# Kernel tuning notes

Measured on AMD Instinct MI355X. Metric: run time of the kernel, lower is better.

The kernel has to match this reference:

```python
import jax, jax.numpy as jnp
import numpy as np

N_EVENT = 100000
N_TRACE = 20000
E_EE = 1000000
E_ET = 500000
E_TE = 500000
D = 128          # embedding_dim == hidden_dim
OUT = 64         # output_dim
L = 3            # num_layers
NTYPES_EDGES = 3 # edge types
B = 64           # graphs per batch


def setup_inputs() -> dict:
    key = jax.random.key(0)
    ks = jax.random.split(key, 16)
    s = 1.0 / np.sqrt(D)
    inp = {
        "event_ids": jnp.arange(N_EVENT, dtype=jnp.int64 if jax.config.jax_enable_x64 else jnp.int32),
        "trace_ids": jnp.arange(N_TRACE, dtype=jnp.int64 if jax.config.jax_enable_x64 else jnp.int32),
        "e2e_src": jax.random.randint(ks[0], (E_EE,), 0, N_EVENT),
        "e2e_dst": jax.random.randint(ks[1], (E_EE,), 0, N_EVENT),
        "e2t_src": jax.random.randint(ks[2], (E_ET,), 0, N_EVENT),
        "e2t_dst": jax.random.randint(ks[3], (E_ET,), 0, N_TRACE),
        "t2e_src": jax.random.randint(ks[4], (E_TE,), 0, N_TRACE),
        "t2e_dst": jax.random.randint(ks[5], (E_TE,), 0, N_EVENT),
        "event_batch": jnp.sort(jax.random.randint(ks[6], (N_EVENT,), 0, B)),
        "trace_batch": jnp.sort(jax.random.randint(ks[7], (N_TRACE,), 0, B)),
        # learned parameters
        "emb_event": jax.random.normal(ks[8], (N_EVENT, D), jnp.float32),
        "emb_trace": jax.random.normal(ks[9], (N_TRACE, D), jnp.float32),
        # per-layer, per-edge-type SAGEConv weights: lin_l (neighbor, with bias), lin_r (root, no bias)
        "Wl": jax.random.normal(ks[10], (L, NTYPES_EDGES, D, D), jnp.float32) * s,
        "bl": jnp.zeros((L, NTYPES_EDGES, D), jnp.float32),
        "Wr": jax.random.normal(ks[11], (L, NTYPES_EDGES, D, D), jnp.float32) * s,
        # output MLP head
        "W1": jax.random.normal(ks[12], (D, D), jnp.float32) * s,
        "b1": jnp.zeros((D,), jnp.float32),
        "W2": jax.random.normal(ks[13], (OUT, D), jnp.float32) * s,
        "b2": jnp.zeros((OUT,), jnp.float32),
    }
    return inp


def reference(event_ids, trace_ids, e2e_src, e2e_dst, e2t_src, e2t_dst,
              t2e_src, t2e_dst, event_batch, trace_batch,
              emb_event, emb_trace, Wl, bl, Wr, W1, b1, W2, b2):
    def seg_mean(x_src, src, dst, n_dst):
        # mean-aggregate source features onto destination nodes (SAGEConv default aggr)
        s = jax.ops.segment_sum(x_src[src], dst, num_segments=n_dst)
        c = jax.ops.segment_sum(jnp.ones(dst.shape, x_src.dtype), dst, num_segments=n_dst)
        return s / jnp.maximum(c, 1.0)[:, None]

    # per-node-type embedding lookup
    x = {"event": emb_event[event_ids], "trace": emb_trace[trace_ids]}
    n = {"event": event_ids.shape[0], "trace": trace_ids.shape[0]}
    # edge types: (src_type, dst_type, src_idx, dst_idx), conv index matches Wl/bl/Wr axis 1
    edges = [
        ("event", "event", e2e_src, e2e_dst),
        ("event", "trace", e2t_src, e2t_dst),
        ("trace", "event", t2e_src, t2e_dst),
    ]
    n_layers = Wl.shape[0]
    for l in range(n_layers):
        new = {k: jnp.zeros((n[k], Wl.shape[-2]), x[k].dtype) for k in x}
        for i, (st, dt, s_idx, d_idx) in enumerate(edges):
            m = seg_mean(x[st], s_idx, d_idx, n[dt])
            # SAGEConv: lin_l(mean neighbors) + lin_r(root); HeteroConv aggr='sum' across edge types
            new[dt] = new[dt] + m @ Wl[l, i].T + bl[l, i] + x[dt] @ Wr[l, i].T
        x = new
    # global_add_pool per node type, then stack+sum over node types
    pooled = (jax.ops.segment_sum(x["event"], event_batch, num_segments=B)
              + jax.ops.segment_sum(x["trace"], trace_batch, num_segments=B))
    h = jax.nn.relu(pooled @ W1.T + b1)
    return h @ W2.T + b2
```

## Files before the change

### kernel.cpp

```cpp
#include <hip/hip_runtime.h>
#include <hip/hip_bf16.h>


#define D 128
#define NB 64
#define OUTD 64
#define NLAY 3

typedef __bf16 bf16;
typedef __bf16 bf16x4 __attribute__((ext_vector_type(4)));
typedef __bf16 bf16x8 __attribute__((ext_vector_type(8)));
typedef float  f32x16 __attribute__((ext_vector_type(16)));

#define LOAD16_TO_LDS(gp, lp) \
    __builtin_amdgcn_global_load_lds((const __attribute__((address_space(1))) void*)(gp), \
                                     (__attribute__((address_space(3))) void*)(lp), 16, 0, 0)

__global__ void gather_all(const float* __restrict__ embE, const int* __restrict__ idsE,
                           bf16* __restrict__ xE, int nE,
                           const float* __restrict__ embT, const int* __restrict__ idsT,
                           bf16* __restrict__ xT, int nT) {
    int idx = blockIdx.x * blockDim.x + threadIdx.x;
    const float* emb; const int* ids; bf16* x;
    int tE = nE * 32;
    if (idx < tE) { emb = embE; ids = idsE; x = xE; }
    else {
        idx -= tE;
        if (idx >= nT * 32) return;
        emb = embT; ids = idsT; x = xT;
    }
    int r = idx >> 5, v = idx & 31;
    float4 f = ((const float4*)(emb + (size_t)ids[r] * D))[v];
    bf16x4 o;
    o[0] = (bf16)f.x; o[1] = (bf16)f.y; o[2] = (bf16)f.z; o[3] = (bf16)f.w;
    ((bf16x4*)(x + (size_t)r * D))[v] = o;
}

__global__ void hist_all(const int* __restrict__ dEE, const int* __restrict__ dET,
                         const int* __restrict__ dTE, int nEE, int nET, int nTE,
                         int* __restrict__ degEE, int* __restrict__ degET, int* __restrict__ degTE,
                         int* __restrict__ rkEE, int* __restrict__ rkET, int* __restrict__ rkTE) {
    int e = blockIdx.x * blockDim.x + threadIdx.x;
    const int* dst; int* deg; int* rk;
    if (e < nEE) { dst = dEE; deg = degEE; rk = rkEE; }
    else {
        e -= nEE;
        if (e < nET) { dst = dET; deg = degET; rk = rkET; }
        else {
            e -= nET;
            if (e >= nTE) return;
            dst = dTE; deg = degTE; rk = rkTE;
        }
    }
    rk[e] = atomicAdd(&deg[dst[e]], 1);
}

__global__ void scan_p1_all(const int* __restrict__ dA, int* __restrict__ oA, int* __restrict__ sA, int nA,
                            const int* __restrict__ dB, int* __restrict__ oB, int* __restrict__ sB, int nB,
                            const int* __restrict__ dC, int* __restrict__ oC, int* __restrict__ sC, int nC) {
    int nbA = (nA + 1023) >> 10, nbB = (nB + 1023) >> 10;
    int b = blockIdx.x;
    const int* deg; int* off; int* bsum; int n; int lb;
    if (b < nbA) { deg = dA; off = oA; bsum = sA; n = nA; lb = b; }
    else if (b < nbA + nbB) { deg = dB; off = oB; bsum = sB; n = nB; lb = b - nbA; }
    else { deg = dC; off = oC; bsum = sC; n = nC; lb = b - nbA - nbB; }
    __shared__ int s[256];
    int t = threadIdx.x;
    int base = lb * 1024 + t * 4;
    int v[4];
    #pragma unroll
    for (int i = 0; i < 4; ++i) v[i] = (base + i < n) ? deg[base + i] : 0;
    int tot = v[0] + v[1] + v[2] + v[3];
    s[t] = tot;
    __syncthreads();
    for (int st = 1; st < 256; st <<= 1) {
        int x = (t >= st) ? s[t - st] : 0;
        __syncthreads();
        s[t] += x;
        __syncthreads();
    }
    int run = s[t] - tot;
    #pragma unroll
    for (int i = 0; i < 4; ++i) {
        if (base + i < n) off[base + i] = run;
        run += v[i];
    }
    if (t == 255) bsum[lb] = s[255];
}

__global__ void scan_p2_all(int* __restrict__ sA, int nbA,
                            int* __restrict__ sB, int nbB,
                            int* __restrict__ sC, int nbC) {
    int* bsum; int nb;
    if (blockIdx.x == 0) { bsum = sA; nb = nbA; }
    else if (blockIdx.x == 1) { bsum = sB; nb = nbB; }
    else { bsum = sC; nb = nbC; }
    __shared__ int s[256];
    int t = threadIdx.x;
    int v = (t < nb) ? bsum[t] : 0;
    s[t] = v;
    __syncthreads();
    for (int st = 1; st < 256; st <<= 1) {
        int x = (t >= st) ? s[t - st] : 0;
        __syncthreads();
        s[t] += x;
        __syncthreads();
    }
    if (t < nb) bsum[t] = s[t] - v;
    if (t == 0) bsum[nb] = s[255];
}

__global__ void scan_p3_all(int* __restrict__ oA, const int* __restrict__ sA, int nA,
                            int* __restrict__ oB, const int* __restrict__ sB, int nB,
                            int* __restrict__ oC, const int* __restrict__ sC, int nC) {
    int cbA = (nA + 255) >> 8, cbB = (nB + 255) >> 8;
    int b = blockIdx.x;
    int* off; const int* bsum; int n; int lb;
    if (b < cbA) { off = oA; bsum = sA; n = nA; lb = b; }
    else if (b < cbA + cbB) { off = oB; bsum = sB; n = nB; lb = b - cbA; }
    else { off = oC; bsum = sC; n = nC; lb = b - cbA - cbB; }
    int i = lb * 256 + threadIdx.x;
    if (i < n) off[i] += bsum[i >> 10];
    if (i == 0) off[n] = bsum[(n + 1023) >> 10];
}

__global__ void adj_fill_all(const int* __restrict__ sEE, const int* __restrict__ dEE, int nEE,
                             const int* __restrict__ sET, const int* __restrict__ dET, int nET,
                             const int* __restrict__ sTE, const int* __restrict__ dTE, int nTE,
                             const int* __restrict__ oEE, const int* __restrict__ oET,
                             const int* __restrict__ oTE,
                             const int* __restrict__ rkEE, const int* __restrict__ rkET,
                             const int* __restrict__ rkTE,
                             int* __restrict__ adjEE, int* __restrict__ adjET,
                             int* __restrict__ adjTE) {
    int e = blockIdx.x * blockDim.x + threadIdx.x;
    const int* src; const int* dst; const int* off; const int* rk; int* adj;
    if (e < nEE) { src = sEE; dst = dEE; off = oEE; rk = rkEE; adj = adjEE; }
    else {
        e -= nEE;
        if (e < nET) { src = sET; dst = dET; off = oET; rk = rkET; adj = adjET; }
        else {
            e -= nET;
            if (e >= nTE) return;
            src = sTE; dst = dTE; off = oTE; rk = rkTE; adj = adjTE;
        }
    }
    adj[off[dst[e]] + rk[e]] = src[e];
}

__global__ void agg_all(const bf16* __restrict__ xE, const bf16* __restrict__ xT,
                        const int* __restrict__ offEE, const int* __restrict__ adjEE,
                        const int* __restrict__ offTE, const int* __restrict__ adjTE,
                        const int* __restrict__ offET, const int* __restrict__ adjET,
                        bf16* __restrict__ mEE, bf16* __restrict__ mTE, bf16* __restrict__ mET,
                        int nE, int nT) {
    int gw = (blockIdx.x * blockDim.x + threadIdx.x) >> 6;
    int lane = threadIdx.x & 63;
    int qE = (nE + 3) >> 2, qT = (nT + 3) >> 2;
    const bf16* xsrc; const int* off; const int* adj; bf16* out; int ndst;
    if (gw < qE) { xsrc = xE; off = offEE; adj = adjEE; out = mEE; ndst = nE; }
    else if (gw < 2 * qE) { gw -= qE; xsrc = xT; off = offTE; adj = adjTE; out = mTE; ndst = nE; }
    else {
        gw -= 2 * qE;
        if (gw >= qT) return;
        xsrc = xE; off = offET; adj = adjET; out = mET; ndst = nT;
    }
    int sub = lane >> 4;
    int sl  = lane & 15;
    int row = gw * 4 + sub;
    if (row >= ndst) row = ndst - 1;
    int s0 = off[row], s1 = off[row + 1];
    float a[8] = {};
    int j = s0;
    for (; j + 8 <= s1; j += 8) {
        int ii[8];
        #pragma unroll
        for (int u = 0; u < 8; ++u) ii[u] = adj[j + u];
        bf16x8 v[8];
        #pragma unroll
        for (int u = 0; u < 8; ++u) v[u] = ((const bf16x8*)(xsrc + (size_t)ii[u] * D))[sl];
        #pragma unroll
        for (int u = 0; u < 8; ++u)
            #pragma unroll
            for (int e = 0; e < 8; ++e) a[e] += (float)v[u][e];
    }
    for (; j + 4 <= s1; j += 4) {
        int i0 = adj[j], i1 = adj[j + 1], i2 = adj[j + 2], i3 = adj[j + 3];
        bf16x8 v0 = ((const bf16x8*)(xsrc + (size_t)i0 * D))[sl];
        bf16x8 v1 = ((const bf16x8*)(xsrc + (size_t)i1 * D))[sl];
        bf16x8 v2 = ((const bf16x8*)(xsrc + (size_t)i2 * D))[sl];
        bf16x8 v3 = ((const bf16x8*)(xsrc + (size_t)i3 * D))[sl];
        #pragma unroll
        for (int e = 0; e < 8; ++e)
            a[e] += (float)v0[e] + (float)v1[e] + (float)v2[e] + (float)v3[e];
    }
    for (; j < s1; ++j) {
        int i0 = adj[j];
        bf16x8 v0 = ((const bf16x8*)(xsrc + (size_t)i0 * D))[sl];
        #pragma unroll
        for (int e = 0; e < 8; ++e) a[e] += (float)v0[e];
    }
    float inv = 1.0f / fmaxf((float)(s1 - s0), 1.0f);
    bf16x8 o;
    #pragma unroll
    for (int e = 0; e < 8; ++e) o[e] = (bf16)(a[e] * inv);
    ((bf16x8*)(out + (size_t)row * D))[sl] = o;
}

__global__ void prep_weights_packed(const float* __restrict__ Wl, const float* __restrict__ Wr,
                                    bf16* __restrict__ wbuf) {
    int idx = blockIdx.x * blockDim.x + threadIdx.x;
    if (idx >= NLAY * 5 * 2048) return;
    int l = idx / (5 * 2048);
    int rem = idx - l * 5 * 2048;
    int mat = rem >> 11;
    int q = rem & 2047;
    int lane = q & 63, t = (q >> 6) & 7, w = q >> 9;
    int r = w * 32 + (lane & 31);
    int c = t * 16 + (lane >> 5) * 8;
    size_t l3 = (size_t)l * 3;
    const float* s0;
    const float* s1 = nullptr;
    switch (mat) {
        case 0: s0 = Wl + (l3 + 0) * D * D; break;
        case 1: s0 = Wl + (l3 + 2) * D * D; break;
        case 2: s0 = Wr + (l3 + 0) * D * D; s1 = Wr + (l3 + 2) * D * D; break;
        case 3: s0 = Wl + (l3 + 1) * D * D; break;
        default: s0 = Wr + (l3 + 1) * D * D; break;
    }
    bf16x8 hi, lo;
    #pragma unroll
    for (int e = 0; e < 8; ++e) {
        float v = s0[r * D + c + e];
        if (s1) v += s1[r * D + c + e];
        bf16 h = (bf16)v;
        hi[e] = h;
        lo[e] = (bf16)(v - (float)h);
    }
    bf16* base = wbuf + (size_t)l * 10 * D * D;
    ((bf16x8*)(base + (size_t)(2 * mat) * D * D))[q] = hi;
    ((bf16x8*)(base + (size_t)(2 * mat + 1) * D * D))[q] = lo;
}

__global__ void prep_bias(const float* __restrict__ bl, float* __restrict__ bbuf) {
    int idx = blockIdx.x * blockDim.x + threadIdx.x;
    if (idx >= NLAY * D) return;
    int l = idx >> 7, o = idx & (D - 1);
    bbuf[l * 2 * D + o]     = bl[(size_t)(l * 3 + 0) * D + o] + bl[(size_t)(l * 3 + 2) * D + o];
    bbuf[l * 2 * D + D + o] = bl[(size_t)(l * 3 + 1) * D + o];
}

__device__ __forceinline__ void gemm_body(const bf16* A0, const bf16* A1, const bf16* A2,
                                          const bf16* Wp, const float* bias, bf16* out,
                                          int M, int nm, int row0, bf16* As) {
    int tid = threadIdx.x;
    int wave = tid >> 6, lane = tid & 63;
    int m = lane & 31, half = lane >> 5;

    f32x16 acc[2];
    #pragma unroll
    for (int rt = 0; rt < 2; ++rt)
        #pragma unroll
        for (int i = 0; i < 16; ++i) acc[rt][i] = 0.f;

    const bf16* Aptr[3] = {A0, A1, A2};
    #pragma unroll
    for (int s = 0; s < 3; ++s) {
        if (s >= nm) break;
        if (s) __syncthreads();
        const bf16* Amat = Aptr[s];
        #pragma unroll
        for (int p = 0; p < 4; ++p) {
            int si = p * 256 + tid;
            int r = si >> 4, u = si & 15;
            int gr = row0 + r; if (gr >= M) gr = M - 1;
            int gc = (u ^ (r & 15)) * 8;
            LOAD16_TO_LDS(Amat + (size_t)gr * D + gc, As + (size_t)(p * 4 + wave) * 512);
        }
        const bf16* wph = Wp + (size_t)(2 * s) * D * D + ((size_t)wave * 512 + lane) * 8;
        const bf16* wpl = wph + D * D;
        bf16x8 bh_c  = *(const bf16x8*)(wph);
        bf16x8 blo_c = *(const bf16x8*)(wpl);
        __syncthreads();

        #pragma unroll 1
        for (int t = 0; t < 8; ++t) {
            bf16x8 bh_n, blo_n;
            if (t < 7) {
                bh_n  = *(const bf16x8*)(wph + (t + 1) * 512);
                blo_n = *(const bf16x8*)(wpl + (t + 1) * 512);
            }
            bf16x8 af[2];
            #pragma unroll
            for (int rt = 0; rt < 2; ++rt) {
                int r = rt * 32 + m;
                int c = t * 2 + half;
                af[rt] = *(const bf16x8*)(As + ((size_t)r * 16 + (c ^ (r & 15))) * 8);
            }
            acc[0] = __builtin_amdgcn_mfma_f32_32x32x16_bf16(af[0], bh_c,  acc[0], 0, 0, 0);
            acc[1] = __builtin_amdgcn_mfma_f32_32x32x16_bf16(af[1], bh_c,  acc[1], 0, 0, 0);
            acc[0] = __builtin_amdgcn_mfma_f32_32x32x16_bf16(af[0], blo_c, acc[0], 0, 0, 0);
            acc[1] = __builtin_amdgcn_mfma_f32_32x32x16_bf16(af[1], blo_c, acc[1], 0, 0, 0);
            bh_c = bh_n; blo_c = blo_n;
        }
    }

    int col = wave * 32 + m;
    float bv = bias[col];
    #pragma unroll
    for (int rt = 0; rt < 2; ++rt) {
        #pragma unroll
        for (int r = 0; r < 16; ++r) {
            int row = row0 + rt * 32 + (r & 3) + 8 * (r >> 2) + 4 * half;
            if (row < M) out[(size_t)row * D + col] = (bf16)(acc[rt][r] + bv);
        }
    }
}

__global__ __launch_bounds__(256) void gemm_all(const bf16* __restrict__ eA0, const bf16* __restrict__ eA1,
                                                const bf16* __restrict__ eA2, const bf16* __restrict__ eW,
                                                const float* __restrict__ eB, bf16* __restrict__ eOut,
                                                int Me, int bE,
                                                const bf16* __restrict__ tA0, const bf16* __restrict__ tA1,
                                                const bf16* __restrict__ tW, const float* __restrict__ tB,
                                                bf16* __restrict__ tOut, int Mt) {
    __shared__ bf16 As[64 * 128];
    if ((int)blockIdx.x < bE)
        gemm_body(eA0, eA1, eA2, eW, eB, eOut, Me, 3, blockIdx.x * 64, As);
    else
        gemm_body(tA0, tA1, (const bf16*)nullptr, tW, tB, tOut, Mt, 2,
                  ((int)blockIdx.x - bE) * 64, As);
}

__global__ void pool_all(const bf16* __restrict__ xE, const int* __restrict__ bEv, int nE, int pbE,
                         const bf16* __restrict__ xT, const int* __restrict__ bTr, int nT,
                         float* __restrict__ pooled) {
    int c = threadIdx.x;
    int blk = blockIdx.x;
    const bf16* x; const int* batch; int n, r0;
    if (blk < pbE) { x = xE; batch = bEv; n = nE; r0 = blk * 64; }
    else { x = xT; batch = bTr; n = nT; r0 = (blk - pbE) * 64; }
    int r1 = min(r0 + 64, n);
    if (r0 >= r1) return;
    int cur = batch[r0];
    float acc = 0.f;
    for (int r = r0; r < r1; ++r) {
        int b = batch[r];
        if (b != cur) { atomicAdd(&pooled[cur * D + c], acc); acc = 0.f; cur = b; }
        acc += (float)x[(size_t)r * D + c];
    }
    atomicAdd(&pooled[cur * D + c], acc);
}

__global__ void head_kernel(const float* __restrict__ pooled, const float* __restrict__ W1,
                            const float* __restrict__ b1, const float* __restrict__ W2,
                            const float* __restrict__ b2, float* __restrict__ out) {
    __shared__ float p[D];
    __shared__ float h[D];
    int b = blockIdx.x, t = threadIdx.x;
    p[t] = pooled[b * D + t];
    __syncthreads();
    float s = b1[t];
    const float* w = W1 + (size_t)t * D;
    #pragma unroll 4
    for (int k = 0; k < D; ++k) s += p[k] * w[k];
    h[t] = fmaxf(s, 0.f);
    __syncthreads();
    if (t < OUTD) {
        float s2 = b2[t];
        const float* w2 = W2 + (size_t)t * D;
        #pragma unroll 4
        for (int k = 0; k < D; ++k) s2 += h[k] * w2[k];
        out[b * OUTD + t] = s2;
    }
}

extern "C" void kernel_launch(void* const* d_in, const int* in_sizes, int n_in,
                              void* d_out, int out_size, void* d_ws, size_t ws_size,
                              hipStream_t stream) {
    const int* event_ids   = (const int*)d_in[0];
    const int* trace_ids   = (const int*)d_in[1];
    const int* e2e_src     = (const int*)d_in[2];
    const int* e2e_dst     = (const int*)d_in[3];
    const int* e2t_src     = (const int*)d_in[4];
    const int* e2t_dst     = (const int*)d_in[5];
    const int* t2e_src     = (const int*)d_in[6];
    const int* t2e_dst     = (const int*)d_in[7];
    const int* event_batch = (const int*)d_in[8];
    const int* trace_batch = (const int*)d_in[9];
    const float* emb_event = (const float*)d_in[10];
    const float* emb_trace = (const float*)d_in[11];
    const float* Wl        = (const float*)d_in[12];
    const float* bl        = (const float*)d_in[13];
    const float* Wr        = (const float*)d_in[14];
    const float* W1        = (const float*)d_in[15];
    const float* b1        = (const float*)d_in[16];
    const float* W2        = (const float*)d_in[17];
    const float* b2        = (const float*)d_in[18];

    const int NE = in_sizes[0];
    const int NT = in_sizes[1];
    const int EE = in_sizes[2];
    const int ET = in_sizes[4];
    const int TE = in_sizes[6];

    size_t cur = 0;
    auto alloc = [&](size_t bytes) -> void* {
        cur = (cur + 255) & ~(size_t)255;
        void* p = (char*)d_ws + cur;
        cur += bytes;
        return p;
    };
    bf16* x_event   = (bf16*)alloc((size_t)NE * D * 2);
    bf16* x_trace   = (bf16*)alloc((size_t)NT * D * 2);
    bf16* nx_event  = (bf16*)alloc((size_t)NE * D * 2);
    bf16* nx_trace  = (bf16*)alloc((size_t)NT * D * 2);
    bf16* m_ee      = (bf16*)alloc((size_t)NE * D * 2);
    bf16* m_te      = (bf16*)alloc((size_t)NE * D * 2);
    bf16* m_et      = (bf16*)alloc((size_t)NT * D * 2);
    float* pooled   = (float*)alloc((size_t)NB * D * 4);
    bf16* wbuf      = (bf16*)alloc((size_t)NLAY * 10 * D * D * 2);
    float* bbuf     = (float*)alloc((size_t)NLAY * 2 * D * 4);
    int* zbase  = (int*)alloc(((size_t)NE + NT + NE) * 4);
    int* deg_ee = zbase;
    int* deg_et = deg_ee + NE;
    int* deg_te = deg_et + NT;
    int* off_ee = (int*)alloc((size_t)(NE + 1) * 4);
    int* adj_ee = (int*)alloc((size_t)EE * 4);
    int* off_et = (int*)alloc((size_t)(NT + 1) * 4);
    int* adj_et = (int*)alloc((size_t)ET * 4);
    int* off_te = (int*)alloc((size_t)(NE + 1) * 4);
    int* adj_te = (int*)alloc((size_t)TE * 4);
    int* bsum_ee = (int*)alloc(((size_t)(NE + 1023) / 1024 + 1) * 4);
    int* bsum_et = (int*)alloc(((size_t)(NT + 1023) / 1024 + 1) * 4);
    int* bsum_te = (int*)alloc(((size_t)(NE + 1023) / 1024 + 1) * 4);
    int* rk_ee = (int*)m_ee;
    int* rk_et = (int*)m_te;
    int* rk_te = (int*)m_et;
    (void)ws_size; (void)n_in; (void)out_size;

    const int nbE = (NE + 1023) / 1024;
    const int nbT = (NT + 1023) / 1024;

    hipMemsetAsync(zbase, 0, ((size_t)NE + NT + NE) * 4, stream);

    gather_all<<<((NE + NT) * 32 + 255) / 256, 256, 0, stream>>>(
        emb_event, event_ids, x_event, NE, emb_trace, trace_ids, x_trace, NT);

    prep_weights_packed<<<(NLAY * 5 * 2048 + 255) / 256, 256, 0, stream>>>(Wl, Wr, wbuf);
    prep_bias<<<(NLAY * D + 255) / 256, 256, 0, stream>>>(bl, bbuf);

    hist_all<<<(EE + ET + TE + 255) / 256, 256, 0, stream>>>(
        e2e_dst, e2t_dst, t2e_dst, EE, ET, TE,
        deg_ee, deg_et, deg_te, rk_ee, rk_et, rk_te);
    scan_p1_all<<<nbE + nbT + nbE, 256, 0, stream>>>(
        deg_ee, off_ee, bsum_ee, NE, deg_et, off_et, bsum_et, NT, deg_te, off_te, bsum_te, NE);
    scan_p2_all<<<3, 256, 0, stream>>>(bsum_ee, nbE, bsum_et, nbT, bsum_te, nbE);
    scan_p3_all<<<((NE + 255) >> 8) * 2 + ((NT + 255) >> 8), 256, 0, stream>>>(
        off_ee, bsum_ee, NE, off_et, bsum_et, NT, off_te, bsum_te, NE);
    adj_fill_all<<<(EE + ET + TE + 255) / 256, 256, 0, stream>>>(
        e2e_src, e2e_dst, EE, e2t_src, e2t_dst, ET, t2e_src, t2e_dst, TE,
        off_ee, off_et, off_te, rk_ee, rk_et, rk_te, adj_ee, adj_et, adj_te);

    const int qE = (NE + 3) >> 2, qT = (NT + 3) >> 2;
    const int aggBlocks = (2 * qE + qT + 3) / 4;
    const int bE = (NE + 63) / 64, bT = (NT + 63) / 64;
    for (int l = 0; l < NLAY; ++l) {
        const bf16* wl_ev = wbuf + (size_t)l * 10 * D * D;
        const bf16* wl_tr = wl_ev + (size_t)6 * D * D;
        const float* be = bbuf + (size_t)l * 2 * D;
        const float* bt = be + D;

        agg_all<<<aggBlocks, 256, 0, stream>>>(x_event, x_trace,
                                               off_ee, adj_ee, off_te, adj_te, off_et, adj_et,
                                               m_ee, m_te, m_et, NE, NT);
        gemm_all<<<bE + bT, 256, 0, stream>>>(m_ee, m_te, x_event, wl_ev, be, nx_event, NE, bE,
                                              m_et, x_trace, wl_tr, bt, nx_trace, NT);

        bf16* t;
        t = x_event; x_event = nx_event; nx_event = t;
        t = x_trace; x_trace = nx_trace; nx_trace = t;
    }

    hipMemsetAsync(pooled, 0, (size_t)NB * D * 4, stream);
    const int pbE = (NE + 63) / 64, pbT = (NT + 63) / 64;
    pool_all<<<pbE + pbT, D, 0, stream>>>(x_event, event_batch, NE, pbE,
                                          x_trace, trace_batch, NT, pooled);

    head_kernel<<<NB, D, 0, stream>>>(pooled, W1, b1, W2, b2, (float*)d_out);
}
```

Measured before the change: 660.3 us.

## Fold last-layer linear transform into pooling via linearity of sum-pool

```diff
diff --git a/kernel.cpp b/kernel.cpp
--- a/kernel.cpp
+++ b/kernel.cpp
@@ -145,7 +145,7 @@
             src = sTE; dst = dTE; off = oTE; rk = rkTE; adj = adjTE;
         }
     }
-    adj[off[dst[e]] + rk[e]] = src[e];
+    __builtin_nontemporal_store(src[e], &adj[off[dst[e]] + rk[e]]);
 }
 
 __global__ void agg_all(const bf16* __restrict__ xE, const bf16* __restrict__ xT,
@@ -332,45 +332,86 @@
                   ((int)blockIdx.x - bE) * 64, As);
 }
 
-__global__ void pool_all(const bf16* __restrict__ xE, const int* __restrict__ bEv, int nE, int pbE,
-                         const bf16* __restrict__ xT, const int* __restrict__ bTr, int nT,
-                         float* __restrict__ pooled) {
+__global__ void pool_m_all(const bf16* __restrict__ m_ee, const bf16* __restrict__ m_te,
+                           const bf16* __restrict__ xE, const bf16* __restrict__ m_et,
+                           const bf16* __restrict__ xT,
+                           const int* __restrict__ bEv, const int* __restrict__ bTr,
+                           int nE, int nT, int pbE, int pbT,
+                           float* __restrict__ pooled5, int* __restrict__ cntE,
+                           int* __restrict__ cntT) {
     int c = threadIdx.x;
     int blk = blockIdx.x;
-    const bf16* x; const int* batch; int n, r0;
-    if (blk < pbE) { x = xE; batch = bEv; n = nE; r0 = blk * 64; }
-    else { x = xT; batch = bTr; n = nT; r0 = (blk - pbE) * 64; }
+    const bf16* x; const int* batch; int n, r0, s;
+    if (blk < 3 * pbE) {
+        s = blk / pbE; int lb = blk - s * pbE;
+        x = (s == 0) ? m_ee : (s == 1) ? m_te : xE;
+        batch = bEv; n = nE; r0 = lb * 64;
+    } else {
+        int q = blk - 3 * pbE;
+        s = 3 + q / pbT; int lb = q - (s - 3) * pbT;
+        x = (s == 3) ? m_et : xT;
+        batch = bTr; n = nT; r0 = lb * 64;
+    }
     int r1 = min(r0 + 64, n);
     if (r0 >= r1) return;
+    float* P = pooled5 + (size_t)s * NB * D;
+    int* cnt = (s == 2) ? cntE : (s == 4) ? cntT : nullptr;
     int cur = batch[r0];
     float acc = 0.f;
+    int run = 0;
     for (int r = r0; r < r1; ++r) {
         int b = batch[r];
-        if (b != cur) { atomicAdd(&pooled[cur * D + c], acc); acc = 0.f; cur = b; }
+        if (b != cur) {
+            atomicAdd(&P[cur * D + c], acc);
+            if (cnt && c == 0) atomicAdd(&cnt[cur], run);
+            acc = 0.f; run = 0; cur = b;
+        }
         acc += (float)x[(size_t)r * D + c];
-    }
-    atomicAdd(&pooled[cur * D + c], acc);
-}
-
-__global__ void head_kernel(const float* __restrict__ pooled, const float* __restrict__ W1,
-                            const float* __restrict__ b1, const float* __restrict__ W2,
-                            const float* __restrict__ b2, float* __restrict__ out) {
-    __shared__ float p[D];
-    __shared__ float h[D];
+        run++;
+    }
+    atomicAdd(&P[cur * D + c], acc);
+    if (cnt && c == 0) atomicAdd(&cnt[cur], run);
+}
+
+__global__ void tail_kernel(const float* __restrict__ pooled5, const int* __restrict__ cntE,
+                            const int* __restrict__ cntT,
+                            const float* __restrict__ Wl, const float* __restrict__ Wr,
+                            const float* __restrict__ bl,
+                            const float* __restrict__ W1, const float* __restrict__ b1,
+                            const float* __restrict__ W2, const float* __restrict__ b2,
+                            float* __restrict__ out) {
+    __shared__ float p5[5][D];
+    __shared__ float hp[D];
+    __shared__ float hh[D];
     int b = blockIdx.x, t = threadIdx.x;
-    p[t] = pooled[b * D + t];
+    #pragma unroll
+    for (int s = 0; s < 5; ++s) p5[s][t] = pooled5[(size_t)(s * NB + b) * D + t];
     __syncthreads();
-    float s = b1[t];
-    const float* w = W1 + (size_t)t * D;
+    float ce = (float)cntE[b], ct = (float)cntT[b];
+    float s = ce * (bl[6 * D + t] + bl[8 * D + t]) + ct * bl[7 * D + t];
+    const float* w0  = Wl + (size_t)6 * D * D + (size_t)t * D;
+    const float* w2  = Wl + (size_t)8 * D * D + (size_t)t * D;
+    const float* wr0 = Wr + (size_t)6 * D * D + (size_t)t * D;
+    const float* wr2 = Wr + (size_t)8 * D * D + (size_t)t * D;
+    const float* w1m = Wl + (size_t)7 * D * D + (size_t)t * D;
+    const float* wr1 = Wr + (size_t)7 * D * D + (size_t)t * D;
     #pragma unroll 4
-    for (int k = 0; k < D; ++k) s += p[k] * w[k];
-    h[t] = fmaxf(s, 0.f);
+    for (int k = 0; k < D; ++k)
+        s += p5[0][k] * w0[k] + p5[1][k] * w2[k] + p5[2][k] * (wr0[k] + wr2[k])
+           + p5[3][k] * w1m[k] + p5[4][k] * wr1[k];
+    hp[t] = s;
+    __syncthreads();
+    float s1 = b1[t];
+    const float* u = W1 + (size_t)t * D;
+    #pragma unroll 4
+    for (int k = 0; k < D; ++k) s1 += hp[k] * u[k];
+    hh[t] = fmaxf(s1, 0.f);
     __syncthreads();
     if (t < OUTD) {
         float s2 = b2[t];
-        const float* w2 = W2 + (size_t)t * D;
+        const float* v = W2 + (size_t)t * D;
         #pragma unroll 4
-        for (int k = 0; k < D; ++k) s2 += h[k] * w2[k];
+        for (int k = 0; k < D; ++k) s2 += hh[k] * v[k];
         out[b * OUTD + t] = s2;
     }
 }
@@ -418,13 +459,16 @@
     bf16* m_ee      = (bf16*)alloc((size_t)NE * D * 2);
     bf16* m_te      = (bf16*)alloc((size_t)NE * D * 2);
     bf16* m_et      = (bf16*)alloc((size_t)NT * D * 2);
-    float* pooled   = (float*)alloc((size_t)NB * D * 4);
     bf16* wbuf      = (bf16*)alloc((size_t)NLAY * 10 * D * D * 2);
     float* bbuf     = (float*)alloc((size_t)NLAY * 2 * D * 4);
-    int* zbase  = (int*)alloc(((size_t)NE + NT + NE) * 4);
+    size_t zInts = (size_t)NE + NT + NE + 5 * NB * D + 2 * NB;
+    int* zbase  = (int*)alloc(zInts * 4);
     int* deg_ee = zbase;
     int* deg_et = deg_ee + NE;
     int* deg_te = deg_et + NT;
+    float* pooled5 = (float*)(deg_te + NE);
+    int* cntE = (int*)(pooled5 + 5 * NB * D);
+    int* cntT = cntE + NB;
     int* off_ee = (int*)alloc((size_t)(NE + 1) * 4);
     int* adj_ee = (int*)alloc((size_t)EE * 4);
     int* off_et = (int*)alloc((size_t)(NT + 1) * 4);
@@ -442,7 +486,7 @@
     const int nbE = (NE + 1023) / 1024;
     const int nbT = (NT + 1023) / 1024;
 
-    hipMemsetAsync(zbase, 0, ((size_t)NE + NT + NE) * 4, stream);
+    hipMemsetAsync(zbase, 0, zInts * 4, stream);
 
     gather_all<<<((NE + NT) * 32 + 255) / 256, 256, 0, stream>>>(
         emb_event, event_ids, x_event, NE, emb_trace, trace_ids, x_trace, NT);
@@ -466,26 +510,26 @@
     const int aggBlocks = (2 * qE + qT + 3) / 4;
     const int bE = (NE + 63) / 64, bT = (NT + 63) / 64;
     for (int l = 0; l < NLAY; ++l) {
-        const bf16* wl_ev = wbuf + (size_t)l * 10 * D * D;
-        const bf16* wl_tr = wl_ev + (size_t)6 * D * D;
-        const float* be = bbuf + (size_t)l * 2 * D;
-        const float* bt = be + D;
-
         agg_all<<<aggBlocks, 256, 0, stream>>>(x_event, x_trace,
                                                off_ee, adj_ee, off_te, adj_te, off_et, adj_et,
                                                m_ee, m_te, m_et, NE, NT);
-        gemm_all<<<bE + bT, 256, 0, stream>>>(m_ee, m_te, x_event, wl_ev, be, nx_event, NE, bE,
-                                              m_et, x_trace, wl_tr, bt, nx_trace, NT);
-
-        bf16* t;
-        t = x_event; x_event = nx_event; nx_event = t;
-        t = x_trace; x_trace = nx_trace; nx_trace = t;
-    }
-
-    hipMemsetAsync(pooled, 0, (size_t)NB * D * 4, stream);
+        if (l < NLAY - 1) {
+            const bf16* wl_ev = wbuf + (size_t)l * 10 * D * D;
+            const bf16* wl_tr = wl_ev + (size_t)6 * D * D;
+            const float* be = bbuf + (size_t)l * 2 * D;
+            const float* bt = be + D;
+            gemm_all<<<bE + bT, 256, 0, stream>>>(m_ee, m_te, x_event, wl_ev, be, nx_event, NE, bE,
+                                                  m_et, x_trace, wl_tr, bt, nx_trace, NT);
+            bf16* t;
+            t = x_event; x_event = nx_event; nx_event = t;
+            t = x_trace; x_trace = nx_trace; nx_trace = t;
+        }
+    }
+
     const int pbE = (NE + 63) / 64, pbT = (NT + 63) / 64;
-    pool_all<<<pbE + pbT, D, 0, stream>>>(x_event, event_batch, NE, pbE,
-                                          x_trace, trace_batch, NT, pooled);
-
-    head_kernel<<<NB, D, 0, stream>>>(pooled, W1, b1, W2, b2, (float*)d_out);
-}
+    pool_m_all<<<3 * pbE + 2 * pbT, D, 0, stream>>>(m_ee, m_te, x_event, m_et, x_trace,
+                                                    event_batch, trace_batch, NE, NT, pbE, pbT,
+                                                    pooled5, cntE, cntT);
+    tail_kernel<<<NB, D, 0, stream>>>(pooled5, cntE, cntT, Wl, Wr, bl,
+                                      W1, b1, W2, b2, (float*)d_out);
+}
```

After: 684.0 us. 1.04x slower.
